# Performance work log

Measured on AMD Instinct MI355X. Metric: run time of the kernel, lower is better.

Reference implementation:

```python
import jax, jax.numpy as jnp
import numpy as np

BN_EPS = 1e-5


def setup_inputs() -> dict:
    key = jax.random.key(0)
    ks = jax.random.split(key, 6)
    B, C, N = 8, 256, 2048
    C4 = C // 4
    return {
        "x": jax.random.normal(ks[0], (B, C, N), dtype=jnp.float32),
        "wq": jax.random.normal(ks[1], (C4, C), dtype=jnp.float32) * (1.0 / np.sqrt(C)),
        "wv": jax.random.normal(ks[2], (C, C), dtype=jnp.float32) * (1.0 / np.sqrt(C)),
        "bv": jax.random.normal(ks[3], (C,), dtype=jnp.float32) * 0.02,
        "wt": jax.random.normal(ks[4], (C, C), dtype=jnp.float32) * (1.0 / np.sqrt(C)),
        "bt": jax.random.normal(ks[5], (C,), dtype=jnp.float32) * 0.02,
        "gamma": jnp.ones((C,), dtype=jnp.float32),
        "beta": jnp.zeros((C,), dtype=jnp.float32),
    }


def reference(x, wq, wv, bv, wt, bt, gamma, beta):
    # x: [B, C, N]. Conv1d(kernel=1) == per-point matmul.
    # q_conv and k_conv share the same weight in the original, so q == k.
    q = jnp.einsum('oc,bcn->bon', wq, x)            # [B, C/4, N]
    # ||q_i - q_j||_2 via the Gram identity (same math as norm of the diff tensor)
    sq = jnp.sum(q * q, axis=1)                     # [B, N]
    gram = jnp.einsum('bci,bcj->bij', q, q)         # [B, N, N]
    d2 = sq[:, :, None] - 2.0 * gram + sq[:, None, :]
    l2 = jnp.sqrt(jnp.maximum(d2, 0.0))             # [B, N, N]
    attn = jax.nn.softmax(-l2, axis=-1)             # rows = queries i
    v = jnp.einsum('oc,bcn->bon', wv, x) + bv[None, :, None]   # [B, C, N]
    # einsum('bij,bkj->bik') then permute(0,2,1) == contract j directly to [B, C, N]
    x_r = jnp.einsum('bij,bcj->bci', attn, v)       # [B, C, N]
    t = jnp.einsum('oc,bcn->bon', wt, x_r) + bt[None, :, None]
    # BatchNorm1d in training mode: batch stats over (B, N), biased variance
    mean = jnp.mean(t, axis=(0, 2), keepdims=True)
    var = jnp.mean((t - mean) ** 2, axis=(0, 2), keepdims=True)
    bn = gamma[None, :, None] * (t - mean) * jax.lax.rsqrt(var + BN_EPS) + beta[None, :, None]
    return x + jnp.maximum(bn, 0.0)
```

## Files before the change

### kernel.cpp

```cpp
#include <hip/hip_runtime.h>
#include <math.h>

#define BDIM 8
#define CDIM 256
#define C4DIM 64
#define NDIM 2048
#define LOG2E_SQ 2.0813689810056077f
#define NEG_2LOG2E_SQ -4.1627379620112154f

typedef short bf16x8 __attribute__((ext_vector_type(8)));
typedef float f32x4 __attribute__((ext_vector_type(4)));

__device__ inline unsigned cvt_pk(float lo, float hi) {
  unsigned r;
  asm("v_cvt_pk_bf16_f32 %0, %1, %2" : "=v"(r) : "v"(lo), "v"(hi));
  return r;
}
__device__ inline float bflo(unsigned u) {
  u <<= 16; float f; __builtin_memcpy(&f, &u, 4); return f;
}
__device__ inline float bfhi(unsigned u) {
  u &= 0xffff0000u; float f; __builtin_memcpy(&f, &u, 4); return f;
}

__global__ __launch_bounds__(256) void prep_kernel(const float* __restrict__ x,
                                                   const float* __restrict__ wq,
                                                   const float* __restrict__ wv,
                                                   const float* __restrict__ wt,
                                                   short* __restrict__ xT,
                                                   short* __restrict__ wqb,
                                                   short* __restrict__ wvb,
                                                   short* __restrict__ wtb,
                                                   float* __restrict__ bnsum) {
  __shared__ float tile[64][65];
  const int fb = blockIdx.x, t = threadIdx.x;
  if (fb < 1024) {
    const int b = fb >> 7, c0 = ((fb >> 5) & 3) * 64, n0 = (fb & 31) * 64;
    const int cl = t >> 2, ng = (t & 3) * 16;
#pragma unroll
    for (int kk = 0; kk < 4; ++kk) {
      float4 v = *(const float4*)&x[((size_t)(b * CDIM + c0 + cl)) * NDIM + n0 + ng + kk * 4];
      tile[cl][ng + kk * 4 + 0] = v.x; tile[cl][ng + kk * 4 + 1] = v.y;
      tile[cl][ng + kk * 4 + 2] = v.z; tile[cl][ng + kk * 4 + 3] = v.w;
    }
    __syncthreads();
    const int nl = t >> 2, cg = (t & 3) * 16;
    unsigned u[8];
#pragma unroll
    for (int e = 0; e < 8; ++e)
      u[e] = cvt_pk(tile[cg + 2 * e][nl], tile[cg + 2 * e + 1][nl]);
    short* dst = &xT[((size_t)b * NDIM + n0 + nl) * CDIM + c0 + cg];
    *(uint4*)&dst[0] = make_uint4(u[0], u[1], u[2], u[3]);
    *(uint4*)&dst[8] = make_uint4(u[4], u[5], u[6], u[7]);
  } else if (fb < 1168) {
    const int idx = ((fb - 1024) * 256 + t) * 4;
    const float* src; short* dst; int off;
    if (idx < 16384)      { src = wq; dst = wqb; off = idx; }
    else if (idx < 81920) { src = wv; dst = wvb; off = idx - 16384; }
    else                  { src = wt; dst = wtb; off = idx - 81920; }
    float4 v = *(const float4*)&src[off];
    *(uint2*)&dst[off] = make_uint2(cvt_pk(v.x, v.y), cvt_pk(v.z, v.w));
  } else {
    bnsum[t] = 0.f; bnsum[256 + t] = 0.f;
  }
}

template<bool STATS>
__device__ __forceinline__ void gemm128(const short* __restrict__ Wb,
                                        const short* __restrict__ Xt,
                                        const float* __restrict__ bias,
                                        short* __restrict__ OUT,
                                        float* __restrict__ bnsum,
                                        float* __restrict__ bnss,
                                        int b, int n0, int c0, int t) {
  const int w = t >> 6, l = t & 63, il = l & 15, g = l >> 4;
  const int wn = w & 1, wc = w >> 1;
  const size_t arow = (size_t)b * NDIM + n0 + wn * 64;
  const int ccol = c0 + wc * 64;
  f32x4 acc[4][4] = {};
#pragma unroll
  for (int ks = 0; ks < 8; ++ks) {
    const int k0 = ks * 32;
    bf16x8 af[4], bfr[4];
#pragma unroll
    for (int nt = 0; nt < 4; ++nt)
      af[nt] = *(const bf16x8*)&Xt[(arow + nt * 16 + il) * CDIM + k0 + g * 8];
#pragma unroll
    for (int ct = 0; ct < 4; ++ct)
      bfr[ct] = *(const bf16x8*)&Wb[(size_t)(ccol + ct * 16 + il) * CDIM + k0 + g * 8];
#pragma unroll
    for (int nt = 0; nt < 4; ++nt)
#pragma unroll
      for (int ct = 0; ct < 4; ++ct)
        acc[nt][ct] = __builtin_amdgcn_mfma_f32_16x16x32_bf16(af[nt], bfr[ct], acc[nt][ct], 0, 0, 0);
  }
#pragma unroll
  for (int ct = 0; ct < 4; ++ct) {
    const int c = ccol + ct * 16 + il;
    const float bs = bias[c];
    float s = 0.f, ss = 0.f;
#pragma unroll
    for (int nt = 0; nt < 4; ++nt) {
      const int n = n0 + wn * 64 + nt * 16 + g * 4;
      float y0 = acc[nt][ct][0] + bs, y1 = acc[nt][ct][1] + bs;
      float y2 = acc[nt][ct][2] + bs, y3 = acc[nt][ct][3] + bs;
      *(uint2*)&OUT[((size_t)(b * CDIM + c)) * NDIM + n] =
          make_uint2(cvt_pk(y0, y1), cvt_pk(y2, y3));
      if (STATS) {
        s += y0 + y1 + y2 + y3;
        ss += y0 * y0 + y1 * y1 + y2 * y2 + y3 * y3;
      }
    }
    if (STATS) {
      s += __shfl_xor(s, 16, 64);   s += __shfl_xor(s, 32, 64);
      ss += __shfl_xor(ss, 16, 64); ss += __shfl_xor(ss, 32, 64);
      if (l < 16) { atomicAdd(&bnsum[c], s); atomicAdd(&bnss[c], ss); }
    }
  }
}

__global__ __launch_bounds__(256) void qv_gemm(const short* __restrict__ wqb,
                                               const short* __restrict__ wvb,
                                               const short* __restrict__ xT,
                                               const float* __restrict__ bv,
                                               short* __restrict__ qT,
                                               float* __restrict__ sq2,
                                               short* __restrict__ vbf) {
  const int fb = blockIdx.x, t = threadIdx.x;
  if (fb < 256) {
    const int b = fb >> 5, c0 = ((fb >> 4) & 1) * 128, n0 = (fb & 15) * 128;
    gemm128<false>(wvb, xT, bv, vbf, nullptr, nullptr, b, n0, c0, t);
  } else {
    const int f = fb - 256;
    const int b = f >> 5, n0 = (f & 31) * 64;
    const int w = t >> 6, l = t & 63, il = l & 15, g = l >> 4;
    const int nw = n0 + w * 16;
    f32x4 acc[4] = {};
#pragma unroll
    for (int ks = 0; ks < 8; ++ks) {
      const int k0 = ks * 32;
      bf16x8 bx = *(const bf16x8*)&xT[((size_t)b * NDIM + nw + il) * CDIM + k0 + g * 8];
#pragma unroll
      for (int ot = 0; ot < 4; ++ot) {
        bf16x8 aw = *(const bf16x8*)&wqb[(size_t)(ot * 16 + il) * CDIM + k0 + g * 8];
        acc[ot] = __builtin_amdgcn_mfma_f32_16x16x32_bf16(aw, bx, acc[ot], 0, 0, 0);
      }
    }
    float sqs = 0.f;
#pragma unroll
    for (int ot = 0; ot < 4; ++ot) {
      unsigned u0 = cvt_pk(acc[ot][0], acc[ot][1]);
      unsigned u1 = cvt_pk(acc[ot][2], acc[ot][3]);
      *(uint2*)&qT[((size_t)b * NDIM + nw + il) * C4DIM + ot * 16 + g * 4] = make_uint2(u0, u1);
      float f0 = bflo(u0), f1 = bfhi(u0), f2 = bflo(u1), f3 = bfhi(u1);
      sqs += f0 * f0 + f1 * f1 + f2 * f2 + f3 * f3;
    }
    sqs += __shfl_xor(sqs, 16, 64);
    sqs += __shfl_xor(sqs, 32, 64);
    if (l < 16) sq2[(size_t)b * NDIM + nw + l] = sqs * LOG2E_SQ;
  }
}

__global__ __launch_bounds__(256) void attn_mfma(const short* __restrict__ qT,
                                                 const short* __restrict__ Vb16,
                                                 const float* __restrict__ sq2,
                                                 short* __restrict__ xrT) {
  __shared__ __align__(16) short vj[2][128 * 32];
  __shared__ __align__(16) short qj[2][32 * 64];
  __shared__ __align__(16) short wlds[4][16][40];

  const int bid = blockIdx.x;
  const int swz = (bid & 7) * 64 + (bid >> 3);
  const int i0    = (swz & 31) * 64;
  const int chalf = (swz >> 5) & 1;
  const int b     = swz >> 6;

  const int t = threadIdx.x;
  const int w = t >> 6, l = t & 63, il = l & 15, g = l >> 4;

  const short* qTb = qT + (size_t)b * NDIM * C4DIM;
  const short* Vbb = Vb16 + ((size_t)b * CDIM + chalf * 128) * NDIM;
  const float* sqb = sq2 + (size_t)b * NDIM;

  const int iglob = i0 + w * 16 + il;
  const bf16x8 bq0 = *(const bf16x8*)&qTb[(size_t)iglob * C4DIM + g * 8];
  const bf16x8 bq1 = *(const bf16x8*)&qTb[(size_t)iglob * C4DIM + 32 + g * 8];
  const float sqi = sqb[iglob];

  const int vcb = t >> 2, vs = t & 3;
  const int vd0 = vcb * 32 + ((vs ^ ((vcb >> 1) & 3)) << 3);
  const int vd1 = vd0 + 64 * 32;
  const int qrow = t >> 3, qslot = t & 7;
  const int qd = qrow * 64 + ((qslot ^ (qrow & 7)) << 3);

  f32x4 acc[8];
#pragma unroll
  for (int k = 0; k < 8; ++k) acc[k] = {0.f, 0.f, 0.f, 0.f};
  float sumw = 0.f;

  f32x4 sqc0, sqc1;
  {
    bf16x8 vr0 = *(const bf16x8*)&Vbb[(size_t)vcb * NDIM + vs * 8];
    bf16x8 vr1 = *(const bf16x8*)&Vbb[(size_t)(vcb + 64) * NDIM + vs * 8];
    *(bf16x8*)&vj[0][vd0] = vr0;
    *(bf16x8*)&vj[0][vd1] = vr1;
    bf16x8 qr = *(const bf16x8*)&qTb[(size_t)qrow * C4DIM + qslot * 8];
    *(bf16x8*)&qj[0][qd] = qr;
    sqc0 = *(const f32x4*)&sqb[g * 4];
    sqc1 = *(const f32x4*)&sqb[16 + g * 4];
  }
  __syncthreads();

  const int NT = NDIM / 32;
  for (int jt = 0; jt < NT; ++jt) {
    const int p = jt & 1;
    const short* vbuf = &vj[p][0];
    const short* qbuf = &qj[p][0];
    short* vbufN = &vj[p ^ 1][0];
    short* qbufN = &qj[p ^ 1][0];
    const bool has_next = (jt + 1 < NT);
    const int j0n = jt * 32 + 32;

    bf16x8 vr0 = {}, vr1 = {}, qr = {};
    f32x4 sqn0 = {}, sqn1 = {};
    if (has_next) {
      vr0 = *(const bf16x8*)&Vbb[(size_t)vcb * NDIM + j0n + vs * 8];
      vr1 = *(const bf16x8*)&Vbb[(size_t)(vcb + 64) * NDIM + j0n + vs * 8];
      qr  = *(const bf16x8*)&qTb[(size_t)(j0n + qrow) * C4DIM + qslot * 8];
      sqn0 = *(const f32x4*)&sqb[j0n + g * 4];
      sqn1 = *(const f32x4*)&sqb[j0n + 16 + g * 4];
    }

#pragma unroll
    for (int h = 0; h < 2; ++h) {
      const int row = h * 16 + il;
      bf16x8 aJ0 = *(const bf16x8*)&qbuf[row * 64 + ((g ^ (il & 7)) << 3)];
      bf16x8 aJ1 = *(const bf16x8*)&qbuf[row * 64 + (((4 + g) ^ (il & 7)) << 3)];
      f32x4 s = {0.f, 0.f, 0.f, 0.f};
      s = __builtin_amdgcn_mfma_f32_16x16x32_bf16(aJ0, bq0, s, 0, 0, 0);
      s = __builtin_amdgcn_mfma_f32_16x16x32_bf16(aJ1, bq1, s, 0, 0, 0);
      const f32x4 sqh = h ? sqc1 : sqc0;
      float wv[4];
#pragma unroll
      for (int r = 0; r < 4; ++r) {
        float e = fmaxf(fmaf(NEG_2LOG2E_SQ, s[r], sqi + sqh[r]), 0.f);
        wv[r] = __builtin_amdgcn_exp2f(-__builtin_amdgcn_sqrtf(e));
        sumw += wv[r];
      }
      *(uint2*)&wlds[w][il][h * 16 + g * 4] =
          make_uint2(cvt_pk(wv[0], wv[1]), cvt_pk(wv[2], wv[3]));
    }

    const bf16x8 bw = *(const bf16x8*)&wlds[w][il][g * 8];

#pragma unroll
    for (int ctl = 0; ctl < 8; ++ctl) {
      const int lr = ctl * 16 + il;
      bf16x8 aV = *(const bf16x8*)&vbuf[lr * 32 + ((g ^ ((il >> 1) & 3)) << 3)];
      acc[ctl] = __builtin_amdgcn_mfma_f32_16x16x32_bf16(aV, bw, acc[ctl], 0, 0, 0);
    }

    if (has_next) {
      *(bf16x8*)&vbufN[vd0] = vr0;
      *(bf16x8*)&vbufN[vd1] = vr1;
      *(bf16x8*)&qbufN[qd] = qr;
      sqc0 = sqn0; sqc1 = sqn1;
    }
    __syncthreads();
  }

  sumw += __shfl_xor(sumw, 16, 64);
  sumw += __shfl_xor(sumw, 32, 64);
  const float inv = 1.f / sumw;
#pragma unroll
  for (int ctl = 0; ctl < 8; ++ctl) {
    float y0 = acc[ctl][0] * inv, y1 = acc[ctl][1] * inv;
    float y2 = acc[ctl][2] * inv, y3 = acc[ctl][3] * inv;
    *(uint2*)&xrT[((size_t)b * NDIM + iglob) * CDIM + chalf * 128 + ctl * 16 + g * 4] =
        make_uint2(cvt_pk(y0, y1), cvt_pk(y2, y3));
  }
}

__global__ __launch_bounds__(256) void t_gemm(const short* __restrict__ wtb,
                                              const short* __restrict__ xrT,
                                              const float* __restrict__ bt,
                                              short* __restrict__ tbf,
                                              float* __restrict__ bnsum,
                                              float* __restrict__ bnss) {
  gemm128<true>(wtb, xrT, bt, tbf, bnsum, bnss,
                blockIdx.z, blockIdx.x * 128, blockIdx.y * 128, threadIdx.x);
}

__global__ __launch_bounds__(256) void final_kernel(const float* __restrict__ x,
                                                    const short* __restrict__ tbf,
                                                    const float* __restrict__ bnsum,
                                                    const float* __restrict__ bnss,
                                                    const float* __restrict__ gamma,
                                                    const float* __restrict__ beta,
                                                    float* __restrict__ out) {
  const size_t idx = ((size_t)blockIdx.x * 256 + threadIdx.x) << 2;
  const int c = (int)((idx >> 11) & 255);
  const float cnt = (float)(BDIM * NDIM);
  const float mean = bnsum[c] / cnt;
  const float var = fmaxf(bnss[c] / cnt - mean * mean, 0.f);
  const float sc = gamma[c] * rsqrtf(var + 1e-5f);
  const float sh = beta[c] - mean * sc;
  float4 xv = *(const float4*)&x[idx];
  uint2 tu = *(const uint2*)&tbf[idx];
  const float t0 = bflo(tu.x), t1 = bfhi(tu.x), t2 = bflo(tu.y), t3 = bfhi(tu.y);
  float4 r;
  r.x = xv.x + fmaxf(t0 * sc + sh, 0.f);
  r.y = xv.y + fmaxf(t1 * sc + sh, 0.f);
  r.z = xv.z + fmaxf(t2 * sc + sh, 0.f);
  r.w = xv.w + fmaxf(t3 * sc + sh, 0.f);
  *(float4*)&out[idx] = r;
}

extern "C" void kernel_launch(void* const* d_in, const int* in_sizes, int n_in,
                              void* d_out, int out_size, void* d_ws, size_t ws_size,
                              hipStream_t stream) {
  const float* x     = (const float*)d_in[0];
  const float* wq    = (const float*)d_in[1];
  const float* wv    = (const float*)d_in[2];
  const float* bv    = (const float*)d_in[3];
  const float* wt    = (const float*)d_in[4];
  const float* bt    = (const float*)d_in[5];
  const float* gamma = (const float*)d_in[6];
  const float* beta  = (const float*)d_in[7];
  float* out = (float*)d_out;
  char* ws = (char*)d_ws;

  short* xbT   = (short*)(ws);
  short* wqb   = (short*)(ws + ((size_t)9  << 20));
  short* wvb   = (short*)(ws + ((size_t)9  << 20) + (256 << 10));
  short* wtb   = (short*)(ws + ((size_t)9  << 20) + (512 << 10));
  short* qT    = (short*)(ws + ((size_t)10 << 20));
  float* sq2   = (float*)(ws + ((size_t)12 << 20));
  short* vbf   = (short*)(ws + ((size_t)13 << 20));
  short* xrT   = (short*)(ws + ((size_t)22 << 20));
  short* tbf   = vbf;
  float* bnsum = (float*)(ws + ((size_t)31 << 20));
  float* bnss  = bnsum + 256;

  prep_kernel<<<dim3(1169), 256, 0, stream>>>(x, wq, wv, wt, xbT, wqb, wvb, wtb, bnsum);
  qv_gemm<<<dim3(512), 256, 0, stream>>>(wqb, wvb, xbT, bv, qT, sq2, vbf);
  attn_mfma<<<dim3(512), 256, 0, stream>>>(qT, vbf, sq2, xrT);
  t_gemm<<<dim3(16, 2, 8), 256, 0, stream>>>(wtb, xrT, bt, tbf, bnsum, bnss);
  final_kernel<<<dim3(4096), 256, 0, stream>>>(x, tbf, bnsum, bnss, gamma, beta, out);
}
```

Baseline: 103.3 us.

## Split attention block across full channel range and skew gram/PV stages

Each block now covers 32 query rows and all 256 value channels instead of 64 rows and half the channels. The four waves split as two row groups by two j-halves for the distance/softmax weights, and as two row groups by two channel halves for the PV MFMA. This stops the gram and exp work from being computed twice per row, once for each channel half. The loop is software-skewed so the PV for tile j-1 runs while the gram for tile j runs, with double-buffered weight tiles. The cost is twice the V tile in LDS, an extra cross-wave sum reduction through shared memory, and more LDS pressure per block.

After: 108.9 us. +5.4%, slower.

```diff
diff --git a/kernel.cpp b/kernel.cpp
--- a/kernel.cpp
+++ b/kernel.cpp
@@ -165,31 +165,32 @@
                                                  const short* __restrict__ Vb16,
                                                  const float* __restrict__ sq2,
                                                  short* __restrict__ xrT) {
-  __shared__ __align__(16) short vj[2][128 * 32];
+  __shared__ __align__(16) short vj[2][256 * 32];
   __shared__ __align__(16) short qj[2][32 * 64];
-  __shared__ __align__(16) short wlds[4][16][40];
+  __shared__ __align__(16) short wlds[2][2][16][40];
+  __shared__ float sums[2][2][16];
 
   const int bid = blockIdx.x;
   const int swz = (bid & 7) * 64 + (bid >> 3);
-  const int i0    = (swz & 31) * 64;
-  const int chalf = (swz >> 5) & 1;
-  const int b     = swz >> 6;
+  const int i0 = (swz & 63) * 32;
+  const int b  = swz >> 6;
 
   const int t = threadIdx.x;
   const int w = t >> 6, l = t & 63, il = l & 15, g = l >> 4;
+  const int ig = w & 1, h = w >> 1;
+  const int isub = ig, chalf = h;
 
   const short* qTb = qT + (size_t)b * NDIM * C4DIM;
-  const short* Vbb = Vb16 + ((size_t)b * CDIM + chalf * 128) * NDIM;
+  const short* Vbb = Vb16 + (size_t)b * CDIM * NDIM;
   const float* sqb = sq2 + (size_t)b * NDIM;
 
-  const int iglob = i0 + w * 16 + il;
+  const int iglob = i0 + ig * 16 + il;
   const bf16x8 bq0 = *(const bf16x8*)&qTb[(size_t)iglob * C4DIM + g * 8];
   const bf16x8 bq1 = *(const bf16x8*)&qTb[(size_t)iglob * C4DIM + 32 + g * 8];
   const float sqi = sqb[iglob];
 
   const int vcb = t >> 2, vs = t & 3;
-  const int vd0 = vcb * 32 + ((vs ^ ((vcb >> 1) & 3)) << 3);
-  const int vd1 = vd0 + 64 * 32;
+  const int vswz = ((vs ^ ((vcb >> 1) & 3)) << 3);
   const int qrow = t >> 3, qslot = t & 7;
   const int qd = qrow * 64 + ((qslot ^ (qrow & 7)) << 3);
 
@@ -198,80 +199,87 @@
   for (int k = 0; k < 8; ++k) acc[k] = {0.f, 0.f, 0.f, 0.f};
   float sumw = 0.f;
 
-  f32x4 sqc0, sqc1;
+  f32x4 sqc;
   {
-    bf16x8 vr0 = *(const bf16x8*)&Vbb[(size_t)vcb * NDIM + vs * 8];
-    bf16x8 vr1 = *(const bf16x8*)&Vbb[(size_t)(vcb + 64) * NDIM + vs * 8];
-    *(bf16x8*)&vj[0][vd0] = vr0;
-    *(bf16x8*)&vj[0][vd1] = vr1;
     bf16x8 qr = *(const bf16x8*)&qTb[(size_t)qrow * C4DIM + qslot * 8];
     *(bf16x8*)&qj[0][qd] = qr;
-    sqc0 = *(const f32x4*)&sqb[g * 4];
-    sqc1 = *(const f32x4*)&sqb[16 + g * 4];
+    sqc = *(const f32x4*)&sqb[h * 16 + g * 4];
   }
   __syncthreads();
 
   const int NT = NDIM / 32;
-  for (int jt = 0; jt < NT; ++jt) {
+#pragma unroll 2
+  for (int jt = 0; jt <= NT; ++jt) {
     const int p = jt & 1;
-    const short* vbuf = &vj[p][0];
-    const short* qbuf = &qj[p][0];
-    short* vbufN = &vj[p ^ 1][0];
-    short* qbufN = &qj[p ^ 1][0];
-    const bool has_next = (jt + 1 < NT);
-    const int j0n = jt * 32 + 32;
-
-    bf16x8 vr0 = {}, vr1 = {}, qr = {};
-    f32x4 sqn0 = {}, sqn1 = {};
-    if (has_next) {
-      vr0 = *(const bf16x8*)&Vbb[(size_t)vcb * NDIM + j0n + vs * 8];
-      vr1 = *(const bf16x8*)&Vbb[(size_t)(vcb + 64) * NDIM + j0n + vs * 8];
-      qr  = *(const bf16x8*)&qTb[(size_t)(j0n + qrow) * C4DIM + qslot * 8];
-      sqn0 = *(const f32x4*)&sqb[j0n + g * 4];
-      sqn1 = *(const f32x4*)&sqb[j0n + 16 + g * 4];
-    }
-
-#pragma unroll
-    for (int h = 0; h < 2; ++h) {
+    const bool do_gram = (jt < NT);
+    const bool do_pv = (jt > 0);
+    const bool next_q = (jt + 1 < NT);
+
+    bf16x8 vr0 = {}, vr1 = {}, vr2 = {}, vr3 = {}, qr = {};
+    f32x4 sqn = {};
+    if (do_gram) {
+      const int j0 = jt * 32;
+      vr0 = *(const bf16x8*)&Vbb[(size_t)vcb * NDIM + j0 + vs * 8];
+      vr1 = *(const bf16x8*)&Vbb[(size_t)(vcb + 64) * NDIM + j0 + vs * 8];
+      vr2 = *(const bf16x8*)&Vbb[(size_t)(vcb + 128) * NDIM + j0 + vs * 8];
+      vr3 = *(const bf16x8*)&Vbb[(size_t)(vcb + 192) * NDIM + j0 + vs * 8];
+    }
+    if (next_q) {
+      const int j0n = jt * 32 + 32;
+      qr = *(const bf16x8*)&qTb[(size_t)(j0n + qrow) * C4DIM + qslot * 8];
+      sqn = *(const f32x4*)&sqb[j0n + h * 16 + g * 4];
+    }
+
+    if (do_gram) {
+      const short* qbuf = &qj[p][0];
       const int row = h * 16 + il;
       bf16x8 aJ0 = *(const bf16x8*)&qbuf[row * 64 + ((g ^ (il & 7)) << 3)];
       bf16x8 aJ1 = *(const bf16x8*)&qbuf[row * 64 + (((4 + g) ^ (il & 7)) << 3)];
       f32x4 s = {0.f, 0.f, 0.f, 0.f};
       s = __builtin_amdgcn_mfma_f32_16x16x32_bf16(aJ0, bq0, s, 0, 0, 0);
       s = __builtin_amdgcn_mfma_f32_16x16x32_bf16(aJ1, bq1, s, 0, 0, 0);
-      const f32x4 sqh = h ? sqc1 : sqc0;
       float wv[4];
 #pragma unroll
       for (int r = 0; r < 4; ++r) {
-        float e = fmaxf(fmaf(NEG_2LOG2E_SQ, s[r], sqi + sqh[r]), 0.f);
+        float e = fmaxf(fmaf(NEG_2LOG2E_SQ, s[r], sqi + sqc[r]), 0.f);
         wv[r] = __builtin_amdgcn_exp2f(-__builtin_amdgcn_sqrtf(e));
         sumw += wv[r];
       }
-      *(uint2*)&wlds[w][il][h * 16 + g * 4] =
+      *(uint2*)&wlds[p][ig][il][h * 16 + g * 4] =
           make_uint2(cvt_pk(wv[0], wv[1]), cvt_pk(wv[2], wv[3]));
     }
 
-    const bf16x8 bw = *(const bf16x8*)&wlds[w][il][g * 8];
-
-#pragma unroll
-    for (int ctl = 0; ctl < 8; ++ctl) {
-      const int lr = ctl * 16 + il;
-      bf16x8 aV = *(const bf16x8*)&vbuf[lr * 32 + ((g ^ ((il >> 1) & 3)) << 3)];
-      acc[ctl] = __builtin_amdgcn_mfma_f32_16x16x32_bf16(aV, bw, acc[ctl], 0, 0, 0);
-    }
-
-    if (has_next) {
-      *(bf16x8*)&vbufN[vd0] = vr0;
-      *(bf16x8*)&vbufN[vd1] = vr1;
-      *(bf16x8*)&qbufN[qd] = qr;
-      sqc0 = sqn0; sqc1 = sqn1;
+    if (do_pv) {
+      const int pp = p ^ 1;
+      const short* vbuf = &vj[pp][0];
+      const bf16x8 bw = *(const bf16x8*)&wlds[pp][isub][il][g * 8];
+#pragma unroll
+      for (int ctl = 0; ctl < 8; ++ctl) {
+        const int lr = chalf * 128 + ctl * 16 + il;
+        bf16x8 aV = *(const bf16x8*)&vbuf[lr * 32 + ((g ^ ((il >> 1) & 3)) << 3)];
+        acc[ctl] = __builtin_amdgcn_mfma_f32_16x16x32_bf16(aV, bw, acc[ctl], 0, 0, 0);
+      }
+    }
+
+    if (do_gram) {
+      short* vbufN = &vj[p][0];
+      *(bf16x8*)&vbufN[(vcb)       * 32 + vswz] = vr0;
+      *(bf16x8*)&vbufN[(vcb + 64)  * 32 + vswz] = vr1;
+      *(bf16x8*)&vbufN[(vcb + 128) * 32 + vswz] = vr2;
+      *(bf16x8*)&vbufN[(vcb + 192) * 32 + vswz] = vr3;
+    }
+    if (next_q) {
+      *(bf16x8*)&qj[p ^ 1][qd] = qr;
+      sqc = sqn;
     }
     __syncthreads();
   }
 
   sumw += __shfl_xor(sumw, 16, 64);
   sumw += __shfl_xor(sumw, 32, 64);
-  const float inv = 1.f / sumw;
+  if (l < 16) sums[ig][h][l] = sumw;
+  __syncthreads();
+  const float inv = 1.f / (sums[isub][0][il] + sums[isub][1][il]);
 #pragma unroll
   for (int ctl = 0; ctl < 8; ++ctl) {
     float y0 = acc[ctl][0] * inv, y1 = acc[ctl][1] * inv;
```

## Split attention channels into quarters to double grid size and occupancy

Applied to the files above, without the earlier changes.

The attention kernel now gives each block 64 output channels instead of 128 and launches 1024 blocks instead of 512. This halves the V tile in LDS and the accumulator registers per block. The aim is more resident waves per CU and better latency hiding. The cost is that QK scores, sqrt and exp are recomputed for twice as many blocks. It also raises wave priority around the PV MFMA loop.

Result: slower. 122.2 us (+18.3%).

```diff
diff --git a/kernel.cpp b/kernel.cpp
--- a/kernel.cpp
+++ b/kernel.cpp
@@ -165,21 +165,21 @@
                                                  const short* __restrict__ Vb16,
                                                  const float* __restrict__ sq2,
                                                  short* __restrict__ xrT) {
-  __shared__ __align__(16) short vj[2][128 * 32];
+  __shared__ __align__(16) short vj[2][64 * 32];
   __shared__ __align__(16) short qj[2][32 * 64];
   __shared__ __align__(16) short wlds[4][16][40];
 
   const int bid = blockIdx.x;
-  const int swz = (bid & 7) * 64 + (bid >> 3);
-  const int i0    = (swz & 31) * 64;
-  const int chalf = (swz >> 5) & 1;
-  const int b     = swz >> 6;
+  const int swz = (bid & 7) * 128 + (bid >> 3);
+  const int i0 = (swz & 31) * 64;
+  const int cq = (swz >> 5) & 3;
+  const int b  = swz >> 7;
 
   const int t = threadIdx.x;
   const int w = t >> 6, l = t & 63, il = l & 15, g = l >> 4;
 
   const short* qTb = qT + (size_t)b * NDIM * C4DIM;
-  const short* Vbb = Vb16 + ((size_t)b * CDIM + chalf * 128) * NDIM;
+  const short* Vbb = Vb16 + ((size_t)b * CDIM + cq * 64) * NDIM;
   const float* sqb = sq2 + (size_t)b * NDIM;
 
   const int iglob = i0 + w * 16 + il;
@@ -188,22 +188,19 @@
   const float sqi = sqb[iglob];
 
   const int vcb = t >> 2, vs = t & 3;
-  const int vd0 = vcb * 32 + ((vs ^ ((vcb >> 1) & 3)) << 3);
-  const int vd1 = vd0 + 64 * 32;
+  const int vd = vcb * 32 + ((vs ^ ((vcb >> 1) & 3)) << 3);
   const int qrow = t >> 3, qslot = t & 7;
   const int qd = qrow * 64 + ((qslot ^ (qrow & 7)) << 3);
 
-  f32x4 acc[8];
-#pragma unroll
-  for (int k = 0; k < 8; ++k) acc[k] = {0.f, 0.f, 0.f, 0.f};
+  f32x4 acc[4];
+#pragma unroll
+  for (int k = 0; k < 4; ++k) acc[k] = {0.f, 0.f, 0.f, 0.f};
   float sumw = 0.f;
 
   f32x4 sqc0, sqc1;
   {
     bf16x8 vr0 = *(const bf16x8*)&Vbb[(size_t)vcb * NDIM + vs * 8];
-    bf16x8 vr1 = *(const bf16x8*)&Vbb[(size_t)(vcb + 64) * NDIM + vs * 8];
-    *(bf16x8*)&vj[0][vd0] = vr0;
-    *(bf16x8*)&vj[0][vd1] = vr1;
+    *(bf16x8*)&vj[0][vd] = vr0;
     bf16x8 qr = *(const bf16x8*)&qTb[(size_t)qrow * C4DIM + qslot * 8];
     *(bf16x8*)&qj[0][qd] = qr;
     sqc0 = *(const f32x4*)&sqb[g * 4];
@@ -214,22 +211,20 @@
   const int NT = NDIM / 32;
   for (int jt = 0; jt < NT; ++jt) {
     const int p = jt & 1;
-    const short* vbuf = &vj[p][0];
-    const short* qbuf = &qj[p][0];
-    short* vbufN = &vj[p ^ 1][0];
-    short* qbufN = &qj[p ^ 1][0];
-    const bool has_next = (jt + 1 < NT);
+    const bool hn = (jt + 1 < NT);
     const int j0n = jt * 32 + 32;
 
-    bf16x8 vr0 = {}, vr1 = {}, qr = {};
+    bf16x8 vr0 = {}, qr = {};
     f32x4 sqn0 = {}, sqn1 = {};
-    if (has_next) {
+    if (hn) {
       vr0 = *(const bf16x8*)&Vbb[(size_t)vcb * NDIM + j0n + vs * 8];
-      vr1 = *(const bf16x8*)&Vbb[(size_t)(vcb + 64) * NDIM + j0n + vs * 8];
       qr  = *(const bf16x8*)&qTb[(size_t)(j0n + qrow) * C4DIM + qslot * 8];
       sqn0 = *(const f32x4*)&sqb[j0n + g * 4];
       sqn1 = *(const f32x4*)&sqb[j0n + 16 + g * 4];
     }
+
+    const short* qbuf = &qj[p][0];
+    const short* vbuf = &vj[p][0];
 
 #pragma unroll
     for (int h = 0; h < 2; ++h) {
@@ -253,17 +248,18 @@
 
     const bf16x8 bw = *(const bf16x8*)&wlds[w][il][g * 8];
 
-#pragma unroll
-    for (int ctl = 0; ctl < 8; ++ctl) {
+    __builtin_amdgcn_s_setprio(1);
+#pragma unroll
+    for (int ctl = 0; ctl < 4; ++ctl) {
       const int lr = ctl * 16 + il;
       bf16x8 aV = *(const bf16x8*)&vbuf[lr * 32 + ((g ^ ((il >> 1) & 3)) << 3)];
       acc[ctl] = __builtin_amdgcn_mfma_f32_16x16x32_bf16(aV, bw, acc[ctl], 0, 0, 0);
     }
-
-    if (has_next) {
-      *(bf16x8*)&vbufN[vd0] = vr0;
-      *(bf16x8*)&vbufN[vd1] = vr1;
-      *(bf16x8*)&qbufN[qd] = qr;
+    __builtin_amdgcn_s_setprio(0);
+
+    if (hn) {
+      *(bf16x8*)&vj[p ^ 1][vd] = vr0;
+      *(bf16x8*)&qj[p ^ 1][qd] = qr;
       sqc0 = sqn0; sqc1 = sqn1;
     }
     __syncthreads();
@@ -273,10 +269,10 @@
   sumw += __shfl_xor(sumw, 32, 64);
   const float inv = 1.f / sumw;
 #pragma unroll
-  for (int ctl = 0; ctl < 8; ++ctl) {
+  for (int ctl = 0; ctl < 4; ++ctl) {
     float y0 = acc[ctl][0] * inv, y1 = acc[ctl][1] * inv;
     float y2 = acc[ctl][2] * inv, y3 = acc[ctl][3] * inv;
-    *(uint2*)&xrT[((size_t)b * NDIM + iglob) * CDIM + chalf * 128 + ctl * 16 + g * 4] =
+    *(uint2*)&xrT[((size_t)b * NDIM + iglob) * CDIM + cq * 64 + ctl * 16 + g * 4] =
         make_uint2(cvt_pk(y0, y1), cvt_pk(y2, y3));
   }
 }
@@ -344,7 +340,7 @@
 
   prep_kernel<<<dim3(1169), 256, 0, stream>>>(x, wq, wv, wt, xbT, wqb, wvb, wtb, bnsum);
   qv_gemm<<<dim3(512), 256, 0, stream>>>(wqb, wvb, xbT, bv, qT, sq2, vbf);
-  attn_mfma<<<dim3(512), 256, 0, stream>>>(qT, vbf, sq2, xrT);
+  attn_mfma<<<dim3(1024), 256, 0, stream>>>(qT, vbf, sq2, xrT);
   t_gemm<<<dim3(16, 2, 8), 256, 0, stream>>>(wtb, xrT, bt, tbf, bnsum, bnss);
   final_kernel<<<dim3(4096), 256, 0, stream>>>(x, tbf, bnsum, bnss, gamma, beta, out);
 }
```

## Software-pipeline attention loop so PV MFMAs overlap next tile's exp math

Applied to the files above, without the earlier changes.

Restructures the attention main loop into a skewed pipeline: iteration jt computes the QK scores and exp weights for tile jt while running the PV MFMAs for tile jt-1, using double-buffered weight LDS. V tiles are loaded and stored one stage later, and the PV MFMA block runs at raised wave priority via s_setprio. The intent is to overlap transcendental VALU work with matrix-core work and to remove the intra-iteration dependency between the weight write and the PV read. It adds one extra loop iteration and more LDS and register pressure.

New measurement: 103.0 us, median of 2. No clear change (-0.3%).

```diff
diff --git a/kernel.cpp b/kernel.cpp
--- a/kernel.cpp
+++ b/kernel.cpp
@@ -167,7 +167,7 @@
                                                  short* __restrict__ xrT) {
   __shared__ __align__(16) short vj[2][128 * 32];
   __shared__ __align__(16) short qj[2][32 * 64];
-  __shared__ __align__(16) short wlds[4][16][40];
+  __shared__ __align__(16) short wlds[2][4][16][40];
 
   const int bid = blockIdx.x;
   const int swz = (bid & 7) * 64 + (bid >> 3);
@@ -200,10 +200,6 @@
 
   f32x4 sqc0, sqc1;
   {
-    bf16x8 vr0 = *(const bf16x8*)&Vbb[(size_t)vcb * NDIM + vs * 8];
-    bf16x8 vr1 = *(const bf16x8*)&Vbb[(size_t)(vcb + 64) * NDIM + vs * 8];
-    *(bf16x8*)&vj[0][vd0] = vr0;
-    *(bf16x8*)&vj[0][vd1] = vr1;
     bf16x8 qr = *(const bf16x8*)&qTb[(size_t)qrow * C4DIM + qslot * 8];
     *(bf16x8*)&qj[0][qd] = qr;
     sqc0 = *(const f32x4*)&sqb[g * 4];
@@ -212,59 +208,83 @@
   __syncthreads();
 
   const int NT = NDIM / 32;
-  for (int jt = 0; jt < NT; ++jt) {
+  for (int jt = 0; jt <= NT; ++jt) {
     const int p = jt & 1;
-    const short* vbuf = &vj[p][0];
-    const short* qbuf = &qj[p][0];
-    short* vbufN = &vj[p ^ 1][0];
-    short* qbufN = &qj[p ^ 1][0];
-    const bool has_next = (jt + 1 < NT);
-    const int j0n = jt * 32 + 32;
+    const bool dg = (jt < NT);
+    const bool dp = (jt > 0);
+    const bool nq = (jt + 1 < NT);
 
     bf16x8 vr0 = {}, vr1 = {}, qr = {};
-    f32x4 sqn0 = {}, sqn1 = {};
-    if (has_next) {
-      vr0 = *(const bf16x8*)&Vbb[(size_t)vcb * NDIM + j0n + vs * 8];
-      vr1 = *(const bf16x8*)&Vbb[(size_t)(vcb + 64) * NDIM + j0n + vs * 8];
-      qr  = *(const bf16x8*)&qTb[(size_t)(j0n + qrow) * C4DIM + qslot * 8];
-      sqn0 = *(const f32x4*)&sqb[j0n + g * 4];
-      sqn1 = *(const f32x4*)&sqb[j0n + 16 + g * 4];
-    }
-
-#pragma unroll
-    for (int h = 0; h < 2; ++h) {
-      const int row = h * 16 + il;
-      bf16x8 aJ0 = *(const bf16x8*)&qbuf[row * 64 + ((g ^ (il & 7)) << 3)];
-      bf16x8 aJ1 = *(const bf16x8*)&qbuf[row * 64 + (((4 + g) ^ (il & 7)) << 3)];
-      f32x4 s = {0.f, 0.f, 0.f, 0.f};
-      s = __builtin_amdgcn_mfma_f32_16x16x32_bf16(aJ0, bq0, s, 0, 0, 0);
-      s = __builtin_amdgcn_mfma_f32_16x16x32_bf16(aJ1, bq1, s, 0, 0, 0);
-      const f32x4 sqh = h ? sqc1 : sqc0;
-      float wv[4];
+    f32x4 tn0 = {}, tn1 = {};
+    if (dg) {
+      const int j0 = jt * 32;
+      vr0 = *(const bf16x8*)&Vbb[(size_t)vcb * NDIM + j0 + vs * 8];
+      vr1 = *(const bf16x8*)&Vbb[(size_t)(vcb + 64) * NDIM + j0 + vs * 8];
+    }
+    if (nq) {
+      const int j1 = (jt + 1) * 32;
+      qr  = *(const bf16x8*)&qTb[(size_t)(j1 + qrow) * C4DIM + qslot * 8];
+      tn0 = *(const f32x4*)&sqb[j1 + g * 4];
+      tn1 = *(const f32x4*)&sqb[j1 + 16 + g * 4];
+    }
+
+    f32x4 s0 = {0.f, 0.f, 0.f, 0.f}, s1 = {0.f, 0.f, 0.f, 0.f};
+    if (dg) {
+      const short* qbuf = &qj[p][0];
+      {
+        const int row = il;
+        bf16x8 aJ0 = *(const bf16x8*)&qbuf[row * 64 + ((g ^ (il & 7)) << 3)];
+        bf16x8 aJ1 = *(const bf16x8*)&qbuf[row * 64 + (((4 + g) ^ (il & 7)) << 3)];
+        s0 = __builtin_amdgcn_mfma_f32_16x16x32_bf16(aJ0, bq0, s0, 0, 0, 0);
+        s0 = __builtin_amdgcn_mfma_f32_16x16x32_bf16(aJ1, bq1, s0, 0, 0, 0);
+      }
+      {
+        const int row = 16 + il;
+        bf16x8 aJ0 = *(const bf16x8*)&qbuf[row * 64 + ((g ^ (il & 7)) << 3)];
+        bf16x8 aJ1 = *(const bf16x8*)&qbuf[row * 64 + (((4 + g) ^ (il & 7)) << 3)];
+        s1 = __builtin_amdgcn_mfma_f32_16x16x32_bf16(aJ0, bq0, s1, 0, 0, 0);
+        s1 = __builtin_amdgcn_mfma_f32_16x16x32_bf16(aJ1, bq1, s1, 0, 0, 0);
+      }
+    }
+
+    if (dp) {
+      const int pp = p ^ 1;
+      const short* vbuf = &vj[pp][0];
+      const bf16x8 bw = *(const bf16x8*)&wlds[pp][w][il][g * 8];
+      __builtin_amdgcn_s_setprio(1);
+#pragma unroll
+      for (int ctl = 0; ctl < 8; ++ctl) {
+        const int lr = ctl * 16 + il;
+        bf16x8 aV = *(const bf16x8*)&vbuf[lr * 32 + ((g ^ ((il >> 1) & 3)) << 3)];
+        acc[ctl] = __builtin_amdgcn_mfma_f32_16x16x32_bf16(aV, bw, acc[ctl], 0, 0, 0);
+      }
+      __builtin_amdgcn_s_setprio(0);
+    }
+
+    if (dg) {
+      float wv0[4], wv1[4];
 #pragma unroll
       for (int r = 0; r < 4; ++r) {
-        float e = fmaxf(fmaf(NEG_2LOG2E_SQ, s[r], sqi + sqh[r]), 0.f);
-        wv[r] = __builtin_amdgcn_exp2f(-__builtin_amdgcn_sqrtf(e));
-        sumw += wv[r];
-      }
-      *(uint2*)&wlds[w][il][h * 16 + g * 4] =
-          make_uint2(cvt_pk(wv[0], wv[1]), cvt_pk(wv[2], wv[3]));
-    }
-
-    const bf16x8 bw = *(const bf16x8*)&wlds[w][il][g * 8];
-
-#pragma unroll
-    for (int ctl = 0; ctl < 8; ++ctl) {
-      const int lr = ctl * 16 + il;
-      bf16x8 aV = *(const bf16x8*)&vbuf[lr * 32 + ((g ^ ((il >> 1) & 3)) << 3)];
-      acc[ctl] = __builtin_amdgcn_mfma_f32_16x16x32_bf16(aV, bw, acc[ctl], 0, 0, 0);
-    }
-
-    if (has_next) {
-      *(bf16x8*)&vbufN[vd0] = vr0;
-      *(bf16x8*)&vbufN[vd1] = vr1;
-      *(bf16x8*)&qbufN[qd] = qr;
-      sqc0 = sqn0; sqc1 = sqn1;
+        float e0 = fmaxf(fmaf(NEG_2LOG2E_SQ, s0[r], sqi + sqc0[r]), 0.f);
+        wv0[r] = __builtin_amdgcn_exp2f(-__builtin_amdgcn_sqrtf(e0));
+        sumw += wv0[r];
+        float e1 = fmaxf(fmaf(NEG_2LOG2E_SQ, s1[r], sqi + sqc1[r]), 0.f);
+        wv1[r] = __builtin_amdgcn_exp2f(-__builtin_amdgcn_sqrtf(e1));
+        sumw += wv1[r];
+      }
+      *(uint2*)&wlds[p][w][il][g * 4] =
+          make_uint2(cvt_pk(wv0[0], wv0[1]), cvt_pk(wv0[2], wv0[3]));
+      *(uint2*)&wlds[p][w][il][16 + g * 4] =
+          make_uint2(cvt_pk(wv1[0], wv1[1]), cvt_pk(wv1[2], wv1[3]));
+    }
+
+    if (dg) {
+      *(bf16x8*)&vj[p][vd0] = vr0;
+      *(bf16x8*)&vj[p][vd1] = vr1;
+    }
+    if (nq) {
+      *(bf16x8*)&qj[p ^ 1][qd] = qr;
+      sqc0 = tn0; sqc1 = tn1;
     }
     __syncthreads();
   }
```
